# Kernel optimization log

Hardware: AMD Instinct MI355X
Metric: run time of the kernel (lower is better)

The kernel has to match this reference:

```python
import jax, jax.numpy as jnp
import numpy as np
import math

D_MODEL = 1024
N_HEADS = 16
D_HEAD = 64
NEG = 1e10


def setup_inputs() -> dict:
    key = jax.random.key(0)
    k0, k1, k2, k3, k4 = jax.random.split(key, 5)
    B, T = 4, 2048
    x = jax.random.normal(k0, (B, T, D_MODEL), dtype=jnp.float32)
    s = 0.02
    W_Q = jax.random.normal(k1, (D_MODEL, N_HEADS * D_HEAD), dtype=jnp.float32) * s
    W_K = jax.random.normal(k2, (D_MODEL, N_HEADS * D_HEAD), dtype=jnp.float32) * s
    W_V = jax.random.normal(k3, (D_MODEL, N_HEADS * D_HEAD), dtype=jnp.float32) * s
    W_O = jax.random.normal(k4, (N_HEADS * D_HEAD, D_MODEL), dtype=jnp.float32) * s
    return {"x": x, "W_Q": W_Q, "W_K": W_K, "W_V": W_V, "W_O": W_O}


def reference(x, W_Q, W_K, W_V, W_O):
    B, T, _ = x.shape
    # project and split heads: [B, nh, T, dh]
    def heads(t):
        return t.reshape(B, T, N_HEADS, D_HEAD).transpose(0, 2, 1, 3)
    q = heads(x @ W_Q)
    k = heads(x @ W_K)
    v = heads(x @ W_V)
    scores = jnp.einsum('bhqd,bhkd->bhqk', q, k)  # [B, nh, T, T]
    # faithful to source: tril(scores) - 1e10 * (1 - tril_mask), THEN divide by sqrt(d_head)
    mask = jnp.tril(jnp.ones((T, T), dtype=scores.dtype))
    masked = scores * mask - NEG * (1.0 - mask)
    attn = jax.nn.softmax(masked / math.sqrt(D_HEAD), axis=-1)
    z = jnp.einsum('bhqk,bhkd->bhqd', attn, v)
    z_flat = z.transpose(0, 2, 1, 3).reshape(B, T, N_HEADS * D_HEAD)
    return z_flat @ W_O
```

## Files before the change

### kernel.cpp

```cpp
#include <hip/hip_runtime.h>
#include <cstdint>
#include <cstddef>

#define DEV __device__ __forceinline__

typedef __attribute__((ext_vector_type(8))) short short8;
typedef __attribute__((ext_vector_type(8))) unsigned short ushort8;
typedef __attribute__((ext_vector_type(4))) unsigned short ushortx4;
typedef __attribute__((ext_vector_type(4))) float floatx4;


DEV unsigned short f2bf(float f) {
    union { float f; uint32_t u; } v; v.f = f;
    uint32_t r = v.u + 0x7FFFu + ((v.u >> 16) & 1u);
    return (unsigned short)(r >> 16);
}

DEV void gld16(const void* g, void* l) {
    __builtin_amdgcn_global_load_lds(
        (const __attribute__((address_space(1))) unsigned int*)g,
        (__attribute__((address_space(3))) unsigned int*)l, 16, 0, 0);
}

template<int NIT>
DEV void stage_swz(const unsigned short* g, int ld, unsigned short* lds) {
    int t = threadIdx.x;
#pragma unroll
    for (int i = 0; i < NIT; ++i) {
        int idx = i * 256 + t;
        int r   = idx >> 3;
        int cl  = idx & 7;
        int cs  = cl ^ (r & 7);
        gld16(g + (size_t)r * ld + cs * 8, lds + idx * 8);
    }
}

DEV short8 ld_frag(const unsigned short* lds, int row, int chunk) {
    int c = chunk ^ (row & 7);
    return *(const short8*)(lds + row * 64 + c * 8);
}


__global__ void cvt_x_kernel(const float* __restrict__ x, unsigned short* __restrict__ xb) {
    int i = (blockIdx.x * 256 + threadIdx.x) * 4;
    floatx4 v = *(const floatx4*)(x + i);
    ushortx4 o = { f2bf(v[0]), f2bf(v[1]), f2bf(v[2]), f2bf(v[3]) };
    *(ushortx4*)(xb + i) = o;
}


__global__ void trans_w_kernel(const float* __restrict__ W0, const float* __restrict__ W1,
                               const float* __restrict__ W2, const float* __restrict__ W3,
                               unsigned short* __restrict__ T0, unsigned short* __restrict__ T1,
                               unsigned short* __restrict__ T2, unsigned short* __restrict__ T3) {
    const float* W = (blockIdx.z == 0) ? W0 : (blockIdx.z == 1) ? W1 : (blockIdx.z == 2) ? W2 : W3;
    unsigned short* T = (blockIdx.z == 0) ? T0 : (blockIdx.z == 1) ? T1 : (blockIdx.z == 2) ? T2 : T3;
    __shared__ float tile[32][33];
    int kb = blockIdx.x * 32, nb = blockIdx.y * 32;
    int tx = threadIdx.x & 31, ty = threadIdx.x >> 5;
#pragma unroll
    for (int i = 0; i < 4; ++i)
        tile[ty + i * 8][tx] = W[(size_t)(kb + ty + i * 8) * 1024 + nb + tx];
    __syncthreads();
#pragma unroll
    for (int i = 0; i < 4; ++i)
        T[(size_t)(nb + ty + i * 8) * 1024 + kb + tx] = f2bf(tile[tx][ty + i * 8]);
}


template<int MODE>
__global__ __launch_bounds__(256, 2) void gemm_kernel(
    const unsigned short* __restrict__ A,
    const unsigned short* __restrict__ B0, const unsigned short* __restrict__ B1,
    const unsigned short* __restrict__ B2,
    unsigned short* __restrict__ oq, unsigned short* __restrict__ ok,
    unsigned short* __restrict__ ov, float* __restrict__ of) {
    __shared__ __align__(16) unsigned short Ab[2][128 * 64];
    __shared__ __align__(16) unsigned short Bb[2][128 * 64];
    const int bx = blockIdx.x, by = blockIdx.y, bz = blockIdx.z;
    const unsigned short* Bt = (MODE == 0) ? (bz == 0 ? B0 : (bz == 1 ? B1 : B2)) : B0;
    const int l = threadIdx.x & 63, w = threadIdx.x >> 6;
    const int l16 = l & 15, l4 = l >> 4;
    const int wr = w >> 1, wc = w & 1;
    const int m0 = by * 128, n0 = bx * 128;

    floatx4 acc[4][4];
#pragma unroll
    for (int i = 0; i < 4; ++i)
#pragma unroll
        for (int j = 0; j < 4; ++j) acc[i][j] = (floatx4){0.f, 0.f, 0.f, 0.f};

    const unsigned short* Ag = A + (size_t)m0 * 1024;
    const unsigned short* Bg = Bt + (size_t)n0 * 1024;

    stage_swz<4>(Ag, 1024, Ab[0]);
    stage_swz<4>(Bg, 1024, Bb[0]);
    __syncthreads();

    for (int kt = 0; kt < 16; ++kt) {
        const int cur = kt & 1;
        if (kt < 15) {
            stage_swz<4>(Ag + (kt + 1) * 64, 1024, Ab[cur ^ 1]);
            stage_swz<4>(Bg + (kt + 1) * 64, 1024, Bb[cur ^ 1]);
        }

        short8 af[4][2], bfr[4][2];
#pragma unroll
        for (int mi = 0; mi < 4; ++mi) {
            int row = wr * 64 + mi * 16 + l16;
#pragma unroll
            for (int kc = 0; kc < 2; ++kc) af[mi][kc] = ld_frag(Ab[cur], row, kc * 4 + l4);
        }
#pragma unroll
        for (int ni = 0; ni < 4; ++ni) {
            int row = wc * 64 + ni * 16 + l16;
#pragma unroll
            for (int kc = 0; kc < 2; ++kc) bfr[ni][kc] = ld_frag(Bb[cur], row, kc * 4 + l4);
        }
#pragma unroll
        for (int mi = 0; mi < 4; ++mi)
#pragma unroll
            for (int ni = 0; ni < 4; ++ni) {
                acc[mi][ni] = __builtin_amdgcn_mfma_f32_16x16x32_bf16(af[mi][0], bfr[ni][0], acc[mi][ni], 0, 0, 0);
                acc[mi][ni] = __builtin_amdgcn_mfma_f32_16x16x32_bf16(af[mi][1], bfr[ni][1], acc[mi][ni], 0, 0, 0);
            }
        __syncthreads();
    }

    if (MODE == 0) {
        unsigned short* dst = (bz == 0) ? oq : (bz == 1) ? ok : ov;
#pragma unroll
        for (int mi = 0; mi < 4; ++mi)
#pragma unroll
            for (int ni = 0; ni < 4; ++ni)
#pragma unroll
                for (int r = 0; r < 4; ++r) {
                    int mm = m0 + wr * 64 + mi * 16 + l4 * 4 + r;
                    int nn = n0 + wc * 64 + ni * 16 + l16;
                    int b = mm >> 11, t = mm & 2047, h = nn >> 6, d = nn & 63;
                    dst[(((size_t)(b * 16 + h)) * 2048 + t) * 64 + d] = f2bf(acc[mi][ni][r]);
                }
    } else {
#pragma unroll
        for (int mi = 0; mi < 4; ++mi)
#pragma unroll
            for (int ni = 0; ni < 4; ++ni)
#pragma unroll
                for (int r = 0; r < 4; ++r) {
                    int mm = m0 + wr * 64 + mi * 16 + l4 * 4 + r;
                    int nn = n0 + wc * 64 + ni * 16 + l16;
                    of[(size_t)mm * 1024 + nn] = acc[mi][ni][r];
                }
    }
}


DEV void attn_step(const short8* kf0, const short8* kf1,
                   const unsigned short* __restrict__ Vl,
                   unsigned short* __restrict__ Pl,
                   const short8 qf[2], floatx4 o[4], float sl[4],
                   bool diag, int w, int l16, int l4) {
    floatx4 s[4];
#pragma unroll
    for (int ki = 0; ki < 4; ++ki) {
        floatx4 z4 = (floatx4){0.f, 0.f, 0.f, 0.f};
        z4 = __builtin_amdgcn_mfma_f32_16x16x32_bf16(qf[0], kf0[ki], z4, 0, 0, 0);
        z4 = __builtin_amdgcn_mfma_f32_16x16x32_bf16(qf[1], kf1[ki], z4, 0, 0, 0);
        s[ki] = z4;
    }

    float pv[4][4];
    float psum[4] = {0.f, 0.f, 0.f, 0.f};
#pragma unroll
    for (int ki = 0; ki < 4; ++ki)
#pragma unroll
        for (int r = 0; r < 4; ++r) {
            float val = s[ki][r] * 0.125f;
            if (diag && (ki * 16 + l16) > (w * 16 + l4 * 4 + r)) val = -1.25e9f;
            float p = __expf(val);
            pv[ki][r] = p;
            psum[r] += p;
        }
#pragma unroll
    for (int r = 0; r < 4; ++r) {
        float t0 = psum[r];
        t0 += __shfl_xor(t0, 1);
        t0 += __shfl_xor(t0, 2);
        t0 += __shfl_xor(t0, 4);
        t0 += __shfl_xor(t0, 8);
        sl[r] += t0;
    }

#pragma unroll
    for (int ki = 0; ki < 4; ++ki)
#pragma unroll
        for (int r = 0; r < 4; ++r)
            Pl[(l4 * 4 + r) * 72 + ki * 16 + l16] = f2bf(pv[ki][r]);

    short8 pa0 = *(const short8*)(Pl + l16 * 72 + l4 * 8);
    short8 pa1 = *(const short8*)(Pl + l16 * 72 + 32 + l4 * 8);

#pragma unroll
    for (int di = 0; di < 4; ++di) {
        int vr = di * 16 + l16;
        short8 bv0 = *(const short8*)(Vl + vr * 72 + l4 * 8);
        short8 bv1 = *(const short8*)(Vl + vr * 72 + 32 + l4 * 8);
        o[di] = __builtin_amdgcn_mfma_f32_16x16x32_bf16(pa0, bv0, o[di], 0, 0, 0);
        o[di] = __builtin_amdgcn_mfma_f32_16x16x32_bf16(pa1, bv1, o[di], 0, 0, 0);
    }
}

__global__ __launch_bounds__(256, 2) void attn_kernel(
    const unsigned short* __restrict__ Q, const unsigned short* __restrict__ K,
    const unsigned short* __restrict__ V, unsigned short* __restrict__ Z) {
    __shared__ __align__(16) unsigned short Klds[2][64 * 64];
    __shared__ __align__(16) unsigned short Vlds[2][64 * 72];
    __shared__ __align__(16) unsigned short Plds[4 * 16 * 72];

    const int bh = blockIdx.x;
    const int j  = blockIdx.y;
    const int qta = j, qtb = 31 - j;
    const int l = threadIdx.x & 63, w = threadIdx.x >> 6;
    const int l16 = l & 15, l4 = l >> 4;

    const unsigned short* Qg = Q + (size_t)bh * 2048 * 64;
    const unsigned short* Kg = K + (size_t)bh * 2048 * 64;
    const unsigned short* Vg = V + (size_t)bh * 2048 * 64;

    short8 qfa[2], qfb[2];
    {
        const unsigned short* qrow = Qg + (size_t)(qta * 64 + w * 16 + l16) * 64;
        qfa[0] = *(const short8*)(qrow + l4 * 8);
        qfa[1] = *(const short8*)(qrow + 32 + l4 * 8);
        qrow = Qg + (size_t)(qtb * 64 + w * 16 + l16) * 64;
        qfb[0] = *(const short8*)(qrow + l4 * 8);
        qfb[1] = *(const short8*)(qrow + 32 + l4 * 8);
    }

    floatx4 oa[4], ob[4];
    float sla[4], slb[4];
#pragma unroll
    for (int i = 0; i < 4; ++i) {
        oa[i] = (floatx4){0.f, 0.f, 0.f, 0.f};
        ob[i] = (floatx4){0.f, 0.f, 0.f, 0.f};
        sla[i] = 0.f;   slb[i] = 0.f;
    }

    unsigned short* Pl = Plds + w * 16 * 72;

    stage_swz<2>(Kg, 64, Klds[0]);
    {
        const unsigned short* vrow = Vg + (size_t)l * 64 + w * 16;
        ushort8 v0 = *(const ushort8*)(vrow);
        ushort8 v1 = *(const ushort8*)(vrow + 8);
#pragma unroll
        for (int jj = 0; jj < 8; ++jj) Vlds[0][(w * 16 + jj) * 72 + l] = v0[jj];
#pragma unroll
        for (int jj = 0; jj < 8; ++jj) Vlds[0][(w * 16 + 8 + jj) * 72 + l] = v1[jj];
    }
    __syncthreads();

    for (int kt = 0; kt <= qtb; ++kt) {
        const int cur = kt & 1;
        const bool pf = kt < qtb;
        ushort8 v0, v1;
        if (pf) {
            stage_swz<2>(Kg + (size_t)(kt + 1) * 64 * 64, 64, Klds[cur ^ 1]);
            const unsigned short* vrow = Vg + (size_t)((kt + 1) * 64 + l) * 64 + w * 16;
            v0 = *(const ushort8*)(vrow);
            v1 = *(const ushort8*)(vrow + 8);
        }

        short8 kf0[4], kf1[4];
#pragma unroll
        for (int ki = 0; ki < 4; ++ki) {
            int row = ki * 16 + l16;
            kf0[ki] = ld_frag(Klds[cur], row, l4);
            kf1[ki] = ld_frag(Klds[cur], row, 4 + l4);
        }

        attn_step(kf0, kf1, Vlds[cur], Pl, qfb, ob, slb, kt == qtb, w, l16, l4);
        if (kt <= qta)
            attn_step(kf0, kf1, Vlds[cur], Pl, qfa, oa, sla, kt == qta, w, l16, l4);

        if (pf) {
            unsigned short* Vn = Vlds[cur ^ 1];
#pragma unroll
            for (int jj = 0; jj < 8; ++jj) Vn[(w * 16 + jj) * 72 + l] = v0[jj];
#pragma unroll
            for (int jj = 0; jj < 8; ++jj) Vn[(w * 16 + 8 + jj) * 72 + l] = v1[jj];
        }
        __syncthreads();
    }

    const int b = bh >> 4, h = bh & 15;
#pragma unroll
    for (int di = 0; di < 4; ++di)
#pragma unroll
        for (int r = 0; r < 4; ++r) {
            int qrow = qta * 64 + w * 16 + l4 * 4 + r;
            Z[((size_t)b * 2048 + qrow) * 1024 + h * 64 + di * 16 + l16] = f2bf(oa[di][r] / sla[r]);
            qrow = qtb * 64 + w * 16 + l4 * 4 + r;
            Z[((size_t)b * 2048 + qrow) * 1024 + h * 64 + di * 16 + l16] = f2bf(ob[di][r] / slb[r]);
        }
}


extern "C" void kernel_launch(void* const* d_in, const int* in_sizes, int n_in,
                              void* d_out, int out_size, void* d_ws, size_t ws_size,
                              hipStream_t stream) {
    const float* x  = (const float*)d_in[0];
    const float* WQ = (const float*)d_in[1];
    const float* WK = (const float*)d_in[2];
    const float* WV = (const float*)d_in[3];
    const float* WO = (const float*)d_in[4];
    float* out = (float*)d_out;

    char* ws = (char*)d_ws;
    const size_t MB = 1024 * 1024;
    unsigned short* xb  = (unsigned short*)(ws);
    unsigned short* wqt = (unsigned short*)(ws + 16 * MB);
    unsigned short* wkt = (unsigned short*)(ws + 18 * MB);
    unsigned short* wvt = (unsigned short*)(ws + 20 * MB);
    unsigned short* wot = (unsigned short*)(ws + 22 * MB);
    unsigned short* qb  = (unsigned short*)(ws + 24 * MB);
    unsigned short* kb  = (unsigned short*)(ws + 40 * MB);
    unsigned short* vb  = (unsigned short*)(ws + 56 * MB);
    unsigned short* zb  = xb;

    cvt_x_kernel<<<8192, 256, 0, stream>>>(x, xb);
    trans_w_kernel<<<dim3(32, 32, 4), 256, 0, stream>>>(WQ, WK, WV, WO, wqt, wkt, wvt, wot);
    gemm_kernel<0><<<dim3(8, 64, 3), 256, 0, stream>>>(xb, wqt, wkt, wvt, qb, kb, vb, nullptr);
    attn_kernel<<<dim3(64, 16), 256, 0, stream>>>(qb, kb, vb, zb);
    gemm_kernel<1><<<dim3(8, 64, 1), 256, 0, stream>>>(zb, wot, nullptr, nullptr,
                                                       nullptr, nullptr, nullptr, out);
}
```

Baseline: 285.4 us.

## Keep attention probabilities in registers via transposed MFMA; single-buffer GEMM LDS

The attention kernel now computes S^T = K·Q^T, so each lane holds scores for one query row. The bf16-packed probabilities can then be fed directly as the B operand of the PV MFMA without the per-wave LDS round-trip. V is stored into LDS with a permuted column index so the register-resident P layout matches V's k ordering, and the row-sum reduction needs only two cross-lane shuffles. Separately, the projection GEMM drops LDS double-buffering for a single buffer with two barriers per k-step. This halves its shared memory (possibly raising occupancy) but exposes global-load latency.

```diff
diff --git a/kernel.cpp b/kernel.cpp
--- a/kernel.cpp
+++ b/kernel.cpp
@@ -75,8 +75,8 @@
     const unsigned short* __restrict__ B2,
     unsigned short* __restrict__ oq, unsigned short* __restrict__ ok,
     unsigned short* __restrict__ ov, float* __restrict__ of) {
-    __shared__ __align__(16) unsigned short Ab[2][128 * 64];
-    __shared__ __align__(16) unsigned short Bb[2][128 * 64];
+    __shared__ __align__(16) unsigned short Ab[128 * 64];
+    __shared__ __align__(16) unsigned short Bb[128 * 64];
     const int bx = blockIdx.x, by = blockIdx.y, bz = blockIdx.z;
     const unsigned short* Bt = (MODE == 0) ? (bz == 0 ? B0 : (bz == 1 ? B1 : B2)) : B0;
     const int l = threadIdx.x & 63, w = threadIdx.x >> 6;
@@ -93,29 +93,24 @@
     const unsigned short* Ag = A + (size_t)m0 * 1024;
     const unsigned short* Bg = Bt + (size_t)n0 * 1024;
 
-    stage_swz<4>(Ag, 1024, Ab[0]);
-    stage_swz<4>(Bg, 1024, Bb[0]);
-    __syncthreads();
-
     for (int kt = 0; kt < 16; ++kt) {
-        const int cur = kt & 1;
-        if (kt < 15) {
-            stage_swz<4>(Ag + (kt + 1) * 64, 1024, Ab[cur ^ 1]);
-            stage_swz<4>(Bg + (kt + 1) * 64, 1024, Bb[cur ^ 1]);
-        }
+        __syncthreads();
+        stage_swz<4>(Ag + kt * 64, 1024, Ab);
+        stage_swz<4>(Bg + kt * 64, 1024, Bb);
+        __syncthreads();
 
         short8 af[4][2], bfr[4][2];
 #pragma unroll
         for (int mi = 0; mi < 4; ++mi) {
             int row = wr * 64 + mi * 16 + l16;
 #pragma unroll
-            for (int kc = 0; kc < 2; ++kc) af[mi][kc] = ld_frag(Ab[cur], row, kc * 4 + l4);
+            for (int kc = 0; kc < 2; ++kc) af[mi][kc] = ld_frag(Ab, row, kc * 4 + l4);
         }
 #pragma unroll
         for (int ni = 0; ni < 4; ++ni) {
             int row = wc * 64 + ni * 16 + l16;
 #pragma unroll
-            for (int kc = 0; kc < 2; ++kc) bfr[ni][kc] = ld_frag(Bb[cur], row, kc * 4 + l4);
+            for (int kc = 0; kc < 2; ++kc) bfr[ni][kc] = ld_frag(Bb, row, kc * 4 + l4);
         }
 #pragma unroll
         for (int mi = 0; mi < 4; ++mi)
@@ -124,7 +119,6 @@
                 acc[mi][ni] = __builtin_amdgcn_mfma_f32_16x16x32_bf16(af[mi][0], bfr[ni][0], acc[mi][ni], 0, 0, 0);
                 acc[mi][ni] = __builtin_amdgcn_mfma_f32_16x16x32_bf16(af[mi][1], bfr[ni][1], acc[mi][ni], 0, 0, 0);
             }
-        __syncthreads();
     }
 
     if (MODE == 0) {
@@ -155,59 +149,43 @@
 }
 
 
-DEV void attn_step(const short8* kf0, const short8* kf1,
-                   const unsigned short* __restrict__ Vl,
-                   unsigned short* __restrict__ Pl,
-                   const short8 qf[2], floatx4 o[4], float sl[4],
-                   bool diag, int w, int l16, int l4) {
-    floatx4 s[4];
+DEV void qk_softmax(const short8 kf0[4], const short8 kf1[4], const short8 qf[2],
+                    short8& pb0, short8& pb1, float& sl,
+                    bool diag, int w, int l16, int l4) {
+    floatx4 st[4];
 #pragma unroll
     for (int ki = 0; ki < 4; ++ki) {
         floatx4 z4 = (floatx4){0.f, 0.f, 0.f, 0.f};
-        z4 = __builtin_amdgcn_mfma_f32_16x16x32_bf16(qf[0], kf0[ki], z4, 0, 0, 0);
-        z4 = __builtin_amdgcn_mfma_f32_16x16x32_bf16(qf[1], kf1[ki], z4, 0, 0, 0);
-        s[ki] = z4;
-    }
-
-    float pv[4][4];
-    float psum[4] = {0.f, 0.f, 0.f, 0.f};
+        z4 = __builtin_amdgcn_mfma_f32_16x16x32_bf16(kf0[ki], qf[0], z4, 0, 0, 0);
+        z4 = __builtin_amdgcn_mfma_f32_16x16x32_bf16(kf1[ki], qf[1], z4, 0, 0, 0);
+        st[ki] = z4;
+    }
+
+    float p[4][4];
+    float psum = 0.f;
 #pragma unroll
     for (int ki = 0; ki < 4; ++ki)
 #pragma unroll
         for (int r = 0; r < 4; ++r) {
-            float val = s[ki][r] * 0.125f;
-            if (diag && (ki * 16 + l16) > (w * 16 + l4 * 4 + r)) val = -1.25e9f;
-            float p = __expf(val);
-            pv[ki][r] = p;
-            psum[r] += p;
-        }
+            float val = st[ki][r] * 0.125f;
+            if (diag && (ki * 16 + l4 * 4 + r) > (w * 16 + l16)) val = -1.25e9f;
+            float e = __expf(val);
+            p[ki][r] = e;
+            psum += e;
+        }
+    psum += __shfl_xor(psum, 16);
+    psum += __shfl_xor(psum, 32);
+    sl += psum;
+
+    short8 t0, t1;
 #pragma unroll
     for (int r = 0; r < 4; ++r) {
-        float t0 = psum[r];
-        t0 += __shfl_xor(t0, 1);
-        t0 += __shfl_xor(t0, 2);
-        t0 += __shfl_xor(t0, 4);
-        t0 += __shfl_xor(t0, 8);
-        sl[r] += t0;
-    }
-
-#pragma unroll
-    for (int ki = 0; ki < 4; ++ki)
-#pragma unroll
-        for (int r = 0; r < 4; ++r)
-            Pl[(l4 * 4 + r) * 72 + ki * 16 + l16] = f2bf(pv[ki][r]);
-
-    short8 pa0 = *(const short8*)(Pl + l16 * 72 + l4 * 8);
-    short8 pa1 = *(const short8*)(Pl + l16 * 72 + 32 + l4 * 8);
-
-#pragma unroll
-    for (int di = 0; di < 4; ++di) {
-        int vr = di * 16 + l16;
-        short8 bv0 = *(const short8*)(Vl + vr * 72 + l4 * 8);
-        short8 bv1 = *(const short8*)(Vl + vr * 72 + 32 + l4 * 8);
-        o[di] = __builtin_amdgcn_mfma_f32_16x16x32_bf16(pa0, bv0, o[di], 0, 0, 0);
-        o[di] = __builtin_amdgcn_mfma_f32_16x16x32_bf16(pa1, bv1, o[di], 0, 0, 0);
-    }
+        t0[r]     = (short)f2bf(p[0][r]);
+        t0[4 + r] = (short)f2bf(p[1][r]);
+        t1[r]     = (short)f2bf(p[2][r]);
+        t1[4 + r] = (short)f2bf(p[3][r]);
+    }
+    pb0 = t0; pb1 = t1;
 }
 
 __global__ __launch_bounds__(256, 2) void attn_kernel(
@@ -215,7 +193,6 @@
     const unsigned short* __restrict__ V, unsigned short* __restrict__ Z) {
     __shared__ __align__(16) unsigned short Klds[2][64 * 64];
     __shared__ __align__(16) unsigned short Vlds[2][64 * 72];
-    __shared__ __align__(16) unsigned short Plds[4 * 16 * 72];
 
     const int bh = blockIdx.x;
     const int j  = blockIdx.y;
@@ -226,6 +203,8 @@
     const unsigned short* Qg = Q + (size_t)bh * 2048 * 64;
     const unsigned short* Kg = K + (size_t)bh * 2048 * 64;
     const unsigned short* Vg = V + (size_t)bh * 2048 * 64;
+
+    const int kl = (l & 35) | ((l & 12) << 1) | ((l & 16) >> 2);
 
     short8 qfa[2], qfb[2];
     {
@@ -238,15 +217,12 @@
     }
 
     floatx4 oa[4], ob[4];
-    float sla[4], slb[4];
+    float sla = 0.f, slb = 0.f;
 #pragma unroll
     for (int i = 0; i < 4; ++i) {
         oa[i] = (floatx4){0.f, 0.f, 0.f, 0.f};
         ob[i] = (floatx4){0.f, 0.f, 0.f, 0.f};
-        sla[i] = 0.f;   slb[i] = 0.f;
-    }
-
-    unsigned short* Pl = Plds + w * 16 * 72;
+    }
 
     stage_swz<2>(Kg, 64, Klds[0]);
     {
@@ -254,9 +230,9 @@
         ushort8 v0 = *(const ushort8*)(vrow);
         ushort8 v1 = *(const ushort8*)(vrow + 8);
 #pragma unroll
-        for (int jj = 0; jj < 8; ++jj) Vlds[0][(w * 16 + jj) * 72 + l] = v0[jj];
-#pragma unroll
-        for (int jj = 0; jj < 8; ++jj) Vlds[0][(w * 16 + 8 + jj) * 72 + l] = v1[jj];
+        for (int jj = 0; jj < 8; ++jj) Vlds[0][(w * 16 + jj) * 72 + kl] = v0[jj];
+#pragma unroll
+        for (int jj = 0; jj < 8; ++jj) Vlds[0][(w * 16 + 8 + jj) * 72 + kl] = v1[jj];
     }
     __syncthreads();
 
@@ -279,30 +255,56 @@
             kf1[ki] = ld_frag(Klds[cur], row, 4 + l4);
         }
 
-        attn_step(kf0, kf1, Vlds[cur], Pl, qfb, ob, slb, kt == qtb, w, l16, l4);
-        if (kt <= qta)
-            attn_step(kf0, kf1, Vlds[cur], Pl, qfa, oa, sla, kt == qta, w, l16, l4);
+        short8 pbb0, pbb1, pba0, pba1;
+        qk_softmax(kf0, kf1, qfb, pbb0, pbb1, slb, kt == qtb, w, l16, l4);
+        const bool doA = kt <= qta;
+        if (doA)
+            qk_softmax(kf0, kf1, qfa, pba0, pba1, sla, kt == qta, w, l16, l4);
+
+        const unsigned short* Vl = Vlds[cur];
+#pragma unroll
+        for (int di = 0; di < 4; ++di) {
+            int vr = di * 16 + l16;
+            short8 bv0 = *(const short8*)(Vl + vr * 72 + l4 * 8);
+            short8 bv1 = *(const short8*)(Vl + vr * 72 + 32 + l4 * 8);
+            ob[di] = __builtin_amdgcn_mfma_f32_16x16x32_bf16(bv0, pbb0, ob[di], 0, 0, 0);
+            ob[di] = __builtin_amdgcn_mfma_f32_16x16x32_bf16(bv1, pbb1, ob[di], 0, 0, 0);
+            if (doA) {
+                oa[di] = __builtin_amdgcn_mfma_f32_16x16x32_bf16(bv0, pba0, oa[di], 0, 0, 0);
+                oa[di] = __builtin_amdgcn_mfma_f32_16x16x32_bf16(bv1, pba1, oa[di], 0, 0, 0);
+            }
+        }
 
         if (pf) {
             unsigned short* Vn = Vlds[cur ^ 1];
 #pragma unroll
-            for (int jj = 0; jj < 8; ++jj) Vn[(w * 16 + jj) * 72 + l] = v0[jj];
-#pragma unroll
-            for (int jj = 0; jj < 8; ++jj) Vn[(w * 16 + 8 + jj) * 72 + l] = v1[jj];
+            for (int jj = 0; jj < 8; ++jj) Vn[(w * 16 + jj) * 72 + kl] = v0[jj];
+#pragma unroll
+            for (int jj = 0; jj < 8; ++jj) Vn[(w * 16 + 8 + jj) * 72 + kl] = v1[jj];
         }
         __syncthreads();
     }
 
-    const int b = bh >> 4, h = bh & 15;
-#pragma unroll
-    for (int di = 0; di < 4; ++di)
-#pragma unroll
-        for (int r = 0; r < 4; ++r) {
-            int qrow = qta * 64 + w * 16 + l4 * 4 + r;
-            Z[((size_t)b * 2048 + qrow) * 1024 + h * 64 + di * 16 + l16] = f2bf(oa[di][r] / sla[r]);
-            qrow = qtb * 64 + w * 16 + l4 * 4 + r;
-            Z[((size_t)b * 2048 + qrow) * 1024 + h * 64 + di * 16 + l16] = f2bf(ob[di][r] / slb[r]);
-        }
+    const int b = bh >> 4;
+    const int hh = (bh & 15) * 64;
+    {
+        float inv = 1.f / sla;
+        unsigned short* zp = Z + ((size_t)b * 2048 + qta * 64 + w * 16 + l16) * 1024 + hh;
+#pragma unroll
+        for (int di = 0; di < 4; ++di)
+#pragma unroll
+            for (int r = 0; r < 4; ++r)
+                zp[di * 16 + l4 * 4 + r] = f2bf(oa[di][r] * inv);
+    }
+    {
+        float inv = 1.f / slb;
+        unsigned short* zp = Z + ((size_t)b * 2048 + qtb * 64 + w * 16 + l16) * 1024 + hh;
+#pragma unroll
+        for (int di = 0; di < 4; ++di)
+#pragma unroll
+            for (int r = 0; r < 4; ++r)
+                zp[di * 16 + l4 * 4 + r] = f2bf(ob[di][r] * inv);
+    }
 }
 
 
```

Measured after the change: 259.2 us. 9.2% less time.
